# Kernel optimization log

Hardware: AMD Instinct MI355X
Metric: run time of the kernel (lower is better)

The kernel has to match this reference:

```python
import jax, jax.numpy as jnp
import numpy as np
from jax import lax

# Topology constants (windowed DAG: compute node i, at global index N_IN+i,
# reads the FANIN immediately preceding global node values).
N_IN = 16      # number of input nodes
FANIN = 16     # connections per compute node
N_NODES = 512  # topologically ordered compute nodes (hidden + output)
N_OUT = 64     # last N_OUT nodes in node_order are outputs
BATCH = 32768
T = N_IN + N_NODES  # total node count


def setup_inputs() -> dict:
    key = jax.random.key(0)
    k1, k2, k3, k4 = jax.random.split(key, 4)
    x = jax.random.normal(k1, (BATCH, N_IN), dtype=jnp.float32)
    # weights scaled down so tanh is not fully saturated through 512 layers
    weights = jax.random.normal(k2, (N_NODES, FANIN), dtype=jnp.float32) * 0.25
    biases = jax.random.normal(k3, (N_NODES,), dtype=jnp.float32) * 0.1
    responses = 1.0 + 0.1 * jax.random.normal(k4, (N_NODES,), dtype=jnp.float32)
    # src indices for node i: global indices [i, i+FANIN) (== previous FANIN nodes,
    # since N_IN == FANIN). Shape [N_NODES, FANIN], int32, all in [0, T).
    src_idx = (jnp.arange(N_NODES, dtype=jnp.int32)[:, None]
               + jnp.arange(FANIN, dtype=jnp.int32)[None, :]
               + (N_IN - FANIN))
    return {"x": x, "weights": weights, "biases": biases,
            "responses": responses, "src_idx": src_idx}


def _forward(x, weights, biases, responses, src_idx):
    B = x.shape[0]
    # values buffer [B, T]: inputs first, then compute nodes in topo order
    values0 = jnp.zeros((B, T), dtype=x.dtype).at[:, :N_IN].set(x)

    def body(values, xs):
        i, idx_row, w, b, r = xs
        src_vals = jnp.take(values, idx_row, axis=1)        # [B, FANIN] gather
        agg = src_vals @ w                                   # [B] weighted sum
        out = jnp.tanh(agg + b) * r                          # activation
        values = lax.dynamic_update_slice(values, out[:, None], (0, N_IN + i))
        return values, None

    ii = jnp.arange(N_NODES, dtype=jnp.int32)
    values, _ = lax.scan(body, values0, (ii, src_idx, weights, biases, responses))
    return values[:, T - N_OUT:]  # [B, N_OUT]


def reference(x, weights, biases, responses, src_idx):
    return _forward(x, weights, biases, responses, src_idx)
```

## Files before the change

### kernel.cpp

```cpp
#include <hip/hip_runtime.h>


typedef float v4f __attribute__((ext_vector_type(4)));

constexpr int kNOut     = 64;
constexpr int kBatch    = 32768;
constexpr int kGStrideF = 48;
constexpr int kLdsFloats = (256 + 3) * kGStrideF;
constexpr float kScale  = 2.8853900817779268f;

#define QPERM(X, CTRL) __int_as_float(__builtin_amdgcn_update_dpp(            \
    __float_as_int(X), __float_as_int(X), (CTRL), 0xF, 0xF, false))

#define PREF(S) {                                                             \
    asm volatile(                                                             \
      "ds_read_b128 %0, %5 offset:0\n\t"                                      \
      "ds_read_b128 %1, %5 offset:16\n\t"                                     \
      "ds_read_b128 %2, %5 offset:64\n\t"                                     \
      "ds_read_b128 %3, %5 offset:80\n\t"                                     \
      "ds_read_b128 %4, %5 offset:128"                                        \
      : "=&v"(qa[S]), "=&v"(qb[S]), "=&v"(qc[S]), "=&v"(qd[S]), "=&v"(qm[S])  \
      : "v"(a));                                                              \
    a += kGStrideF * 4; }

#define WAITG(S)                                                              \
    asm volatile("s_waitcnt lgkmcnt(15)"                                      \
      : "+v"(qa[S]), "+v"(qb[S]), "+v"(qc[S]), "+v"(qd[S]), "+v"(qm[S]));

#define NODE1(WLO, WHI, BH, W15, UIN, UOUT, A0,A1,A2,A3,A4,A5,A6,A7) {        \
    float p = fmaf((A0), (WLO).x, (BH));                                      \
    p = fmaf((A1), (WLO).y, p);                                               \
    p = fmaf((A2), (WLO).z, p);                                               \
    p = fmaf((A3), (WLO).w, p);                                               \
    p = fmaf((A4), (WHI).x, p);                                               \
    p = fmaf((A5), (WHI).y, p);                                               \
    p = fmaf((A6), (WHI).z, p);                                               \
    p = fmaf((A7), (WHI).w, p);                                               \
    float s_ = p + QPERM(p, 0xB1);                   \
    float mg = QPERM((A1), 0xB1);                      \
    float acc = fmaf((UIN), (W15), s_);                \
    float exv = __builtin_amdgcn_exp2f(acc);                                  \
    (UOUT) = __builtin_amdgcn_rcpf(exv + 1.0f);                               \
    (A0) = is_l1 ? (UIN) : mg; }

#define GROUP(G, A0,A1,A2,A3,A4,A5,A6,A7) {                                   \
    PREF(((G) + 3) & 3)                                                       \
    WAITG((G) & 3)                                                            \
    NODE1(qa[(G)&3], qb[(G)&3], qm[(G)&3].x, qm[(G)&3].y, u0, u1,             \
          A0,A1,A2,A3,A4,A5,A6,A7)                                            \
    NODE1(qc[(G)&3], qd[(G)&3], qm[(G)&3].z, qm[(G)&3].w, u1, u0,             \
          A1,A2,A3,A4,A5,A6,A7,A0) }

__global__ __launch_bounds__(256) void neat_fwd(
    const float* __restrict__ x,
    const float* __restrict__ w,
    const float* __restrict__ bias,
    const float* __restrict__ resp,
    float* __restrict__ out)
{
    __shared__ alignas(16) float ldsw[kLdsFloats];
    __shared__ float rst[512];

    const int t  = threadIdx.x;
    const int jl = t & 1;
    const bool is_l1 = (jl == 1);

    rst[t] = resp[t];
    rst[t + 256] = resp[t + 256];
    __syncthreads();

    const float4* __restrict__ w4 = reinterpret_cast<const float4*>(w);
    const float m2k = -2.0f * kScale;
    #pragma unroll
    for (int k = 0; k < 2; ++k) {
        int n = t + (k << 8);
        float4 a0 = w4[n*4+0], a1 = w4[n*4+1], a2 = w4[n*4+2], a3 = w4[n*4+3];
        float wv0=a0.x, wv1=a0.y, wv2=a0.z, wv3=a0.w;
        float wv4=a1.x, wv5=a1.y, wv6=a1.z, wv7=a1.w;
        float wv8=a2.x, wv9=a2.y, wv10=a2.z, wv11=a2.w;
        float wv12=a3.x, wv13=a3.y, wv14=a3.z, wv15=a3.w;
        float sum = 0.0f;
        float ws0,ws1,ws2,ws3,ws4,ws5,ws6,ws7,ws8,ws9,ws10,ws11,ws12,ws13,ws14,ws15;
        #define DO(J) { float rho = (n + J < 16) ? 1.0f : rst[n + J - 16];    \
                        float wr = wv##J * rho; sum += wr; ws##J = wr * m2k; }
        DO(0) DO(1) DO(2) DO(3) DO(4) DO(5) DO(6) DO(7)
        DO(8) DO(9) DO(10) DO(11) DO(12) DO(13) DO(14) DO(15)
        #undef DO
        int q = n >> 1, h = n & 1;
        float* gb = ldsw + q * kGStrideF;
        *reinterpret_cast<float4*>(gb + h*16 + 0)  = make_float4(ws0, ws1, ws2, ws3);
        *reinterpret_cast<float4*>(gb + h*16 + 4)  = make_float4(ws4, ws5, ws6, ws7);
        *reinterpret_cast<float4*>(gb + h*16 + 8)  = make_float4(0.0f, ws8, ws9, ws10);
        *reinterpret_cast<float4*>(gb + h*16 + 12) = make_float4(ws11, ws12, ws13, ws14);
        float Bh = (bias[n] + sum) * (kScale * 0.5f);
        gb[32 + h*2] = Bh;  gb[33 + h*2] = ws15;
        gb[40 + h*2] = Bh;  gb[41 + h*2] = ws15;
    }

    const int e = blockIdx.x * 128 + (t >> 1);
    const float4* __restrict__ x4p = reinterpret_cast<const float4*>(x);
    float4 X0 = x4p[e*4+0], X1 = x4p[e*4+1], X2 = x4p[e*4+2], X3 = x4p[e*4+3];
    float xx0 = fmaf(-0.5f, X0.x, 0.5f), xx1 = fmaf(-0.5f, X0.y, 0.5f);
    float xx2 = fmaf(-0.5f, X0.z, 0.5f), xx3 = fmaf(-0.5f, X0.w, 0.5f);
    float xx4 = fmaf(-0.5f, X1.x, 0.5f), xx5 = fmaf(-0.5f, X1.y, 0.5f);
    float xx6 = fmaf(-0.5f, X1.z, 0.5f), xx7 = fmaf(-0.5f, X1.w, 0.5f);
    float xx8 = fmaf(-0.5f, X2.x, 0.5f), xx9 = fmaf(-0.5f, X2.y, 0.5f);
    float xx10 = fmaf(-0.5f, X2.z, 0.5f), xx11 = fmaf(-0.5f, X2.w, 0.5f);
    float xx12 = fmaf(-0.5f, X3.x, 0.5f), xx13 = fmaf(-0.5f, X3.y, 0.5f);
    float xx14 = fmaf(-0.5f, X3.z, 0.5f), xx15 = fmaf(-0.5f, X3.w, 0.5f);
    float r0 = is_l1 ? xx7  : xx0;
    float r1 = is_l1 ? xx8  : xx1;
    float r2 = is_l1 ? xx9  : xx2;
    float r3 = is_l1 ? xx10 : xx3;
    float r4 = is_l1 ? xx11 : xx4;
    float r5 = is_l1 ? xx12 : xx5;
    float r6 = is_l1 ? xx13 : xx6;
    float r7 = is_l1 ? xx14 : xx7;
    float u0 = xx15;
    float u1 = 0.0f;

    const float4* __restrict__ rr4 = reinterpret_cast<const float4*>(resp);
    float* __restrict__ op = out + (size_t)e * kNOut + jl * 8;

    __syncthreads();

    unsigned int a = (unsigned int)(unsigned long long)(&ldsw[0])
                   + (unsigned int)(jl << 5);

    v4f qa[4], qb[4], qc[4], qd[4], qm[4];
    PREF(0) PREF(1) PREF(2)

    #pragma unroll 1
    for (int g = 0; g < 32; ++g) {
        GROUP(0, r0,r1,r2,r3,r4,r5,r6,r7)
        GROUP(1, r2,r3,r4,r5,r6,r7,r0,r1)
        GROUP(2, r4,r5,r6,r7,r0,r1,r2,r3)
        GROUP(3, r6,r7,r0,r1,r2,r3,r4,r5)
        GROUP(4, r0,r1,r2,r3,r4,r5,r6,r7)
        GROUP(5, r2,r3,r4,r5,r6,r7,r0,r1)
        GROUP(6, r4,r5,r6,r7,r0,r1,r2,r3)
        GROUP(7, r6,r7,r0,r1,r2,r3,r4,r5)
        if (g >= 28) {
            int m = g - 28;
            const float4 ra = rr4[112 + 4 * m + 2 * jl];
            const float4 rb = rr4[112 + 4 * m + 2 * jl + 1];
            float o0 = is_l1 ? r1 : r0;
            float o1 = is_l1 ? r2 : r1;
            float o2 = is_l1 ? r3 : r2;
            float o3 = is_l1 ? r4 : r3;
            float o4 = is_l1 ? r5 : r4;
            float o5 = is_l1 ? r6 : r5;
            float o6 = is_l1 ? r7 : r6;
            float o7 = is_l1 ? u0 : r7;
            float4 q0_ = make_float4(fmaf(-2.0f, o0, 1.0f) * ra.x,
                                     fmaf(-2.0f, o1, 1.0f) * ra.y,
                                     fmaf(-2.0f, o2, 1.0f) * ra.z,
                                     fmaf(-2.0f, o3, 1.0f) * ra.w);
            float4 q1_ = make_float4(fmaf(-2.0f, o4, 1.0f) * rb.x,
                                     fmaf(-2.0f, o5, 1.0f) * rb.y,
                                     fmaf(-2.0f, o6, 1.0f) * rb.z,
                                     fmaf(-2.0f, o7, 1.0f) * rb.w);
            *reinterpret_cast<float4*>(op + 16 * m)     = q0_;
            *reinterpret_cast<float4*>(op + 16 * m + 4) = q1_;
        }
    }

    asm volatile("s_waitcnt lgkmcnt(0)" ::: "memory");
}

extern "C" void kernel_launch(void* const* d_in, const int* in_sizes, int n_in,
                              void* d_out, int out_size, void* d_ws, size_t ws_size,
                              hipStream_t stream) {
    const float* x    = (const float*)d_in[0];
    const float* w    = (const float*)d_in[1];
    const float* bias = (const float*)d_in[2];
    const float* resp = (const float*)d_in[3];
    float* out = (float*)d_out;
    dim3 block(256);
    dim3 grid(kBatch / 128);
    hipLaunchKernelGGL(neat_fwd, grid, block, 0, stream, x, w, bias, resp, out);
}
```

Measured before the change: 89.63 us.

## Store per-node weights as fp16 in LDS and prefetch 8-node regions

Weights are now packed as fp16 pairs in LDS, halving the bytes each node's weight fetch needs. The LDS layout is regrouped into 8-node supergroups, and the software pipeline changes from 4-stage per-2-node prefetch to double-buffered 12-read prefetches per 8 nodes. This cuts LDS read instructions and bandwidth per node but adds fp16-to-fp32 conversions in the FMA chain and loses weight precision, which may compound across 512 sequential tanh layers.

```diff
diff --git a/kernel.cpp b/kernel.cpp
--- a/kernel.cpp
+++ b/kernel.cpp
@@ -1,41 +1,62 @@
 #include <hip/hip_runtime.h>
 
 
-typedef float v4f __attribute__((ext_vector_type(4)));
-
-constexpr int kNOut     = 64;
-constexpr int kBatch    = 32768;
-constexpr int kGStrideF = 48;
-constexpr int kLdsFloats = (256 + 3) * kGStrideF;
+typedef float    v4f __attribute__((ext_vector_type(4)));
+typedef _Float16 h8  __attribute__((ext_vector_type(8)));
+
+constexpr int   kNOut   = 64;
+constexpr int   kBatch  = 32768;
+constexpr int   kSgF    = 96;
+constexpr int   kSgB    = 384;
+constexpr int   kLdsFloats = 65 * kSgF;
 constexpr float kScale  = 2.8853900817779268f;
 
 #define QPERM(X, CTRL) __int_as_float(__builtin_amdgcn_update_dpp(            \
     __float_as_int(X), __float_as_int(X), (CTRL), 0xF, 0xF, false))
 
+__device__ __forceinline__ unsigned pack2(float lo, float hi) {
+    _Float16 l = (_Float16)lo, h = (_Float16)hi;
+    unsigned short ul = __builtin_bit_cast(unsigned short, l);
+    unsigned short uh = __builtin_bit_cast(unsigned short, h);
+    return ((unsigned)uh << 16) | ul;
+}
+
 #define PREF(S) {                                                             \
     asm volatile(                                                             \
-      "ds_read_b128 %0, %5 offset:0\n\t"                                      \
-      "ds_read_b128 %1, %5 offset:16\n\t"                                     \
-      "ds_read_b128 %2, %5 offset:64\n\t"                                     \
-      "ds_read_b128 %3, %5 offset:80\n\t"                                     \
-      "ds_read_b128 %4, %5 offset:128"                                        \
-      : "=&v"(qa[S]), "=&v"(qb[S]), "=&v"(qc[S]), "=&v"(qd[S]), "=&v"(qm[S])  \
+      "ds_read_b128 %0, %12 offset:0\n\t"                                     \
+      "ds_read_b128 %1, %12 offset:32\n\t"                                    \
+      "ds_read_b128 %2, %12 offset:64\n\t"                                    \
+      "ds_read_b128 %3, %12 offset:96\n\t"                                    \
+      "ds_read_b128 %4, %12 offset:128\n\t"                                   \
+      "ds_read_b128 %5, %12 offset:160\n\t"                                   \
+      "ds_read_b128 %6, %12 offset:192\n\t"                                   \
+      "ds_read_b128 %7, %12 offset:224\n\t"                                   \
+      "ds_read_b128 %8, %12 offset:256\n\t"                                   \
+      "ds_read_b128 %9, %12 offset:288\n\t"                                   \
+      "ds_read_b128 %10, %12 offset:320\n\t"                                  \
+      "ds_read_b128 %11, %12 offset:352"                                      \
+      : "=&v"(qw0[S]), "=&v"(qw1[S]), "=&v"(qw2[S]), "=&v"(qw3[S]),           \
+        "=&v"(qw4[S]), "=&v"(qw5[S]), "=&v"(qw6[S]), "=&v"(qw7[S]),           \
+        "=&v"(qm0[S]), "=&v"(qm1[S]), "=&v"(qm2[S]), "=&v"(qm3[S])            \
       : "v"(a));                                                              \
-    a += kGStrideF * 4; }
-
-#define WAITG(S)                                                              \
-    asm volatile("s_waitcnt lgkmcnt(15)"                                      \
-      : "+v"(qa[S]), "+v"(qb[S]), "+v"(qc[S]), "+v"(qd[S]), "+v"(qm[S]));
-
-#define NODE1(WLO, WHI, BH, W15, UIN, UOUT, A0,A1,A2,A3,A4,A5,A6,A7) {        \
-    float p = fmaf((A0), (WLO).x, (BH));                                      \
-    p = fmaf((A1), (WLO).y, p);                                               \
-    p = fmaf((A2), (WLO).z, p);                                               \
-    p = fmaf((A3), (WLO).w, p);                                               \
-    p = fmaf((A4), (WHI).x, p);                                               \
-    p = fmaf((A5), (WHI).y, p);                                               \
-    p = fmaf((A6), (WHI).z, p);                                               \
-    p = fmaf((A7), (WHI).w, p);                                               \
+    a += kSgB; }
+
+#define WAITR(S)                                                              \
+    asm volatile("s_waitcnt lgkmcnt(12)"                                      \
+      : "+v"(qw0[S]), "+v"(qw1[S]), "+v"(qw2[S]), "+v"(qw3[S]),               \
+        "+v"(qw4[S]), "+v"(qw5[S]), "+v"(qw6[S]), "+v"(qw7[S]),               \
+        "+v"(qm0[S]), "+v"(qm1[S]), "+v"(qm2[S]), "+v"(qm3[S]));
+
+#define NODE1(QW, BH, W15, UIN, UOUT, A0,A1,A2,A3,A4,A5,A6,A7) {              \
+    h8 wh = __builtin_bit_cast(h8, (QW));                                     \
+    float p = fmaf((A0), (float)wh[0], (BH));                                 \
+    p = fmaf((A1), (float)wh[1], p);                                          \
+    p = fmaf((A2), (float)wh[2], p);                                          \
+    p = fmaf((A3), (float)wh[3], p);                                          \
+    p = fmaf((A4), (float)wh[4], p);                                          \
+    p = fmaf((A5), (float)wh[5], p);                                          \
+    p = fmaf((A6), (float)wh[6], p);                                          \
+    p = fmaf((A7), (float)wh[7], p);                                          \
     float s_ = p + QPERM(p, 0xB1);                   \
     float mg = QPERM((A1), 0xB1);                      \
     float acc = fmaf((UIN), (W15), s_);                \
@@ -43,13 +64,17 @@
     (UOUT) = __builtin_amdgcn_rcpf(exv + 1.0f);                               \
     (A0) = is_l1 ? (UIN) : mg; }
 
-#define GROUP(G, A0,A1,A2,A3,A4,A5,A6,A7) {                                   \
-    PREF(((G) + 3) & 3)                                                       \
-    WAITG((G) & 3)                                                            \
-    NODE1(qa[(G)&3], qb[(G)&3], qm[(G)&3].x, qm[(G)&3].y, u0, u1,             \
-          A0,A1,A2,A3,A4,A5,A6,A7)                                            \
-    NODE1(qc[(G)&3], qd[(G)&3], qm[(G)&3].z, qm[(G)&3].w, u1, u0,             \
-          A1,A2,A3,A4,A5,A6,A7,A0) }
+#define REGION(SP, SC) {                                                      \
+    PREF(SP)                                                                  \
+    WAITR(SC)                                                                 \
+    NODE1(qw0[SC], qm0[SC].x, qm0[SC].y, u0, u1, r0,r1,r2,r3,r4,r5,r6,r7)     \
+    NODE1(qw1[SC], qm0[SC].z, qm0[SC].w, u1, u0, r1,r2,r3,r4,r5,r6,r7,r0)     \
+    NODE1(qw2[SC], qm1[SC].x, qm1[SC].y, u0, u1, r2,r3,r4,r5,r6,r7,r0,r1)     \
+    NODE1(qw3[SC], qm1[SC].z, qm1[SC].w, u1, u0, r3,r4,r5,r6,r7,r0,r1,r2)     \
+    NODE1(qw4[SC], qm2[SC].x, qm2[SC].y, u0, u1, r4,r5,r6,r7,r0,r1,r2,r3)     \
+    NODE1(qw5[SC], qm2[SC].z, qm2[SC].w, u1, u0, r5,r6,r7,r0,r1,r2,r3,r4)     \
+    NODE1(qw6[SC], qm3[SC].x, qm3[SC].y, u0, u1, r6,r7,r0,r1,r2,r3,r4,r5)     \
+    NODE1(qw7[SC], qm3[SC].z, qm3[SC].w, u1, u0, r7,r0,r1,r2,r3,r4,r5,r6) }
 
 __global__ __launch_bounds__(256) void neat_fwd(
     const float* __restrict__ x,
@@ -74,27 +99,30 @@
     #pragma unroll
     for (int k = 0; k < 2; ++k) {
         int n = t + (k << 8);
-        float4 a0 = w4[n*4+0], a1 = w4[n*4+1], a2 = w4[n*4+2], a3 = w4[n*4+3];
-        float wv0=a0.x, wv1=a0.y, wv2=a0.z, wv3=a0.w;
-        float wv4=a1.x, wv5=a1.y, wv6=a1.z, wv7=a1.w;
-        float wv8=a2.x, wv9=a2.y, wv10=a2.z, wv11=a2.w;
-        float wv12=a3.x, wv13=a3.y, wv14=a3.z, wv15=a3.w;
+        const float4* wn = w4 + n * 4;
+        float4 a0 = wn[0], a1 = wn[1], a2 = wn[2], a3 = wn[3];
         float sum = 0.0f;
         float ws0,ws1,ws2,ws3,ws4,ws5,ws6,ws7,ws8,ws9,ws10,ws11,ws12,ws13,ws14,ws15;
-        #define DO(J) { float rho = (n + J < 16) ? 1.0f : rst[n + J - 16];    \
-                        float wr = wv##J * rho; sum += wr; ws##J = wr * m2k; }
-        DO(0) DO(1) DO(2) DO(3) DO(4) DO(5) DO(6) DO(7)
-        DO(8) DO(9) DO(10) DO(11) DO(12) DO(13) DO(14) DO(15)
+        #define DO(J, V) { float rho = (n + (J) < 16) ? 1.0f : rst[n + (J) - 16]; \
+                           float wr = (V) * rho; sum += wr; ws##J = wr * m2k; }
+        DO(0,a0.x)  DO(1,a0.y)  DO(2,a0.z)  DO(3,a0.w)
+        DO(4,a1.x)  DO(5,a1.y)  DO(6,a1.z)  DO(7,a1.w)
+        DO(8,a2.x)  DO(9,a2.y)  DO(10,a2.z) DO(11,a2.w)
+        DO(12,a3.x) DO(13,a3.y) DO(14,a3.z) DO(15,a3.w)
         #undef DO
-        int q = n >> 1, h = n & 1;
-        float* gb = ldsw + q * kGStrideF;
-        *reinterpret_cast<float4*>(gb + h*16 + 0)  = make_float4(ws0, ws1, ws2, ws3);
-        *reinterpret_cast<float4*>(gb + h*16 + 4)  = make_float4(ws4, ws5, ws6, ws7);
-        *reinterpret_cast<float4*>(gb + h*16 + 8)  = make_float4(0.0f, ws8, ws9, ws10);
-        *reinterpret_cast<float4*>(gb + h*16 + 12) = make_float4(ws11, ws12, ws13, ws14);
+        const int sg = n >> 3, s = n & 7;
+        float* gb = ldsw + sg * kSgF;
+        uint4 lo = make_uint4(pack2(ws0, ws1),  pack2(ws2, ws3),
+                              pack2(ws4, ws5),  pack2(ws6, ws7));
+        uint4 hi = make_uint4(pack2(0.0f, ws8), pack2(ws9, ws10),
+                              pack2(ws11,ws12), pack2(ws13,ws14));
+        uint4* dst = reinterpret_cast<uint4*>(gb + s * 8);
+        dst[0] = lo;
+        dst[1] = hi;
         float Bh = (bias[n] + sum) * (kScale * 0.5f);
-        gb[32 + h*2] = Bh;  gb[33 + h*2] = ws15;
-        gb[40 + h*2] = Bh;  gb[41 + h*2] = ws15;
+        int mi = 64 + (s >> 1) * 8 + (s & 1) * 2;
+        gb[mi]     = Bh;  gb[mi + 1] = ws15;
+        gb[mi + 4] = Bh;  gb[mi + 5] = ws15;
     }
 
     const int e = blockIdx.x * 128 + (t >> 1);
@@ -125,21 +153,16 @@
     __syncthreads();
 
     unsigned int a = (unsigned int)(unsigned long long)(&ldsw[0])
-                   + (unsigned int)(jl << 5);
-
-    v4f qa[4], qb[4], qc[4], qd[4], qm[4];
-    PREF(0) PREF(1) PREF(2)
+                   + (unsigned int)(jl << 4);
+
+    v4f qw0[2], qw1[2], qw2[2], qw3[2], qw4[2], qw5[2], qw6[2], qw7[2];
+    v4f qm0[2], qm1[2], qm2[2], qm3[2];
+    PREF(0)
 
     #pragma unroll 1
     for (int g = 0; g < 32; ++g) {
-        GROUP(0, r0,r1,r2,r3,r4,r5,r6,r7)
-        GROUP(1, r2,r3,r4,r5,r6,r7,r0,r1)
-        GROUP(2, r4,r5,r6,r7,r0,r1,r2,r3)
-        GROUP(3, r6,r7,r0,r1,r2,r3,r4,r5)
-        GROUP(4, r0,r1,r2,r3,r4,r5,r6,r7)
-        GROUP(5, r2,r3,r4,r5,r6,r7,r0,r1)
-        GROUP(6, r4,r5,r6,r7,r0,r1,r2,r3)
-        GROUP(7, r6,r7,r0,r1,r2,r3,r4,r5)
+        REGION(1, 0)
+        REGION(0, 1)
         if (g >= 28) {
             int m = g - 28;
             const float4 ra = rr4[112 + 4 * m + 2 * jl];
```

Measured after the change: 85.62 us, median of 2. 1.05x faster.
